# Performance work log

Hardware: AMD Instinct MI355X
Metric: run time of the kernel (lower is better)

Reference implementation:

```python
import jax, jax.numpy as jnp
import numpy as np

OUT_FEATURES = 4096
IN_FEATURES = 4096
NUMEL = OUT_FEATURES * IN_FEATURES          # 16777216
NUM_SUPER = NUMEL // 256                    # 65536 superblocks of 256 weights


def setup_inputs() -> dict:
    key = jax.random.key(0)
    k_x, k_p, k_d, k_dm, k_s, k_m = jax.random.split(key, 6)
    x = jax.random.normal(k_x, (2, 2048, IN_FEATURES), dtype=jnp.float32)
    # packed bytes: two 4-bit quants per byte
    packed = jax.random.randint(k_p, (NUMEL // 2,), 0, 256, dtype=jnp.int32)
    # per-superblock fp scale/min (small positive values like real Q4_K 'd'/'dmin')
    d = jax.random.uniform(k_d, (NUM_SUPER,), dtype=jnp.float32) * 0.02
    dmin = jax.random.uniform(k_dm, (NUM_SUPER,), dtype=jnp.float32) * 0.02
    # per-subblock 6-bit scale/min quants (8 subblocks per superblock)
    scales = jax.random.randint(k_s, (NUM_SUPER * 8,), 0, 64, dtype=jnp.int32)
    mins = jax.random.randint(k_m, (NUM_SUPER * 8,), 0, 64, dtype=jnp.int32)
    return {"x": x, "packed": packed, "d": d, "dmin": dmin,
            "scales": scales, "mins": mins}


def _q4_k_dequantize(packed, d, dmin, scales, mins):
    # nibble split: low then high, interleaved per byte (stack dim=1 + flatten)
    low = packed & 15
    high = (packed >> 4) & 15
    q = jnp.stack([low, high], axis=1).reshape(-1).astype(jnp.float32)  # [NUMEL]
    blocks = q.reshape(NUM_SUPER, 8, 32)
    blk_scale = (scales.astype(jnp.float32) / 63.0).reshape(NUM_SUPER, 8, 1)
    blk_min = (mins.astype(jnp.float32) / 63.0).reshape(NUM_SUPER, 8, 1)
    normalized = blocks / 15.0 * blk_scale + blk_min
    w = normalized * d.reshape(NUM_SUPER, 1, 1) + dmin.reshape(NUM_SUPER, 1, 1)
    return w.reshape(OUT_FEATURES, IN_FEATURES)


def reference(x, packed, d, dmin, scales, mins):
    w = _q4_k_dequantize(packed, d, dmin, scales, mins).astype(x.dtype)
    # F.linear(x, w) = x @ w.T ; bias is None
    return jnp.einsum('bsk,nk->bsn', x, w)
```

## Files before the change

kernel.cpp:

```cpp
#include <hip/hip_runtime.h>
#include <stdint.h>

#define M_DIM 4096
#define K_DIM 4096
#define N_DIM 4096

typedef float f32x4 __attribute__((ext_vector_type(4)));
typedef int   i32x4 __attribute__((ext_vector_type(4)));

__global__ __launch_bounds__(256) void quant_x(const float* __restrict__ x,
                                               int8_t* __restrict__ xq,
                                               float* __restrict__ sx) {
    __shared__ float red[4];
    const int row  = blockIdx.x;
    const int base = threadIdx.x * 16;
    const float* xr = x + (size_t)row * K_DIM + base;
    float4 v[4];
#pragma unroll
    for (int c = 0; c < 4; ++c) v[c] = ((const float4*)xr)[c];
    float am = 0.f;
#pragma unroll
    for (int c = 0; c < 4; ++c) {
        am = fmaxf(am, fabsf(v[c].x)); am = fmaxf(am, fabsf(v[c].y));
        am = fmaxf(am, fabsf(v[c].z)); am = fmaxf(am, fabsf(v[c].w));
    }
#pragma unroll
    for (int off = 32; off; off >>= 1) am = fmaxf(am, __shfl_xor(am, off, 64));
    if ((threadIdx.x & 63) == 0) red[threadIdx.x >> 6] = am;
    __syncthreads();
    float amax = fmaxf(fmaxf(red[0], red[1]), fmaxf(red[2], red[3]));
    amax = fmaxf(amax, 1e-20f);
    const float inv = 127.0f / amax;
    int ow[4];
#pragma unroll
    for (int c = 0; c < 4; ++c) {
        int q0 = __float2int_rn(v[c].x * inv);
        int q1 = __float2int_rn(v[c].y * inv);
        int q2 = __float2int_rn(v[c].z * inv);
        int q3 = __float2int_rn(v[c].w * inv);
        ow[c] = (q0 & 255) | ((q1 & 255) << 8) | ((q2 & 255) << 16) | ((q3 & 255) << 24);
    }
    ((int4*)(xq + (size_t)row * K_DIM + base))[0] = make_int4(ow[0], ow[1], ow[2], ow[3]);
    if (threadIdx.x == 0) sx[row] = amax / 127.0f;
}

__global__ __launch_bounds__(256) void quant_w(const int* __restrict__ packed,
                                               const float* __restrict__ d,
                                               const float* __restrict__ dmin,
                                               const int* __restrict__ scales,
                                               const int* __restrict__ mins,
                                               int8_t* __restrict__ wq,
                                               float* __restrict__ sw) {
    __shared__ float sa[128], sb[128], red[4];
    const int n = blockIdx.x;
    const int t = threadIdx.x;
    float m = 0.f;
    if (t < 128) {
        int sub  = n * 128 + t;
        int sidx = n * 16 + (t >> 3);
        float dd = d[sidx], dm = dmin[sidx];
        float a = dd * (float)scales[sub] * (1.0f / 945.0f);
        float b = dd * (float)mins[sub] * (1.0f / 63.0f) + dm;
        sa[t] = a; sb[t] = b;
        m = 15.0f * a + b;
    }
#pragma unroll
    for (int off = 32; off; off >>= 1) m = fmaxf(m, __shfl_xor(m, off, 64));
    if ((t & 63) == 0) red[t >> 6] = m;
    __syncthreads();
    float rowmax = fmaxf(fmaxf(red[0], red[1]), fmaxf(red[2], red[3]));
    rowmax = fmaxf(rowmax, 1e-20f);
    const float inv = 127.0f / rowmax;

    const int sub = t >> 1;
    const float a = sa[sub] * inv;
    const float b = sb[sub] * inv;
    const int4* p4 = (const int4*)(packed + (size_t)n * (K_DIM / 2) + t * 8);
    int4 pv0 = p4[0], pv1 = p4[1];
    int bytes[8] = {pv0.x, pv0.y, pv0.z, pv0.w, pv1.x, pv1.y, pv1.z, pv1.w};
    int ow[4];
#pragma unroll
    for (int c = 0; c < 4; ++c) {
        int b0 = bytes[2 * c], b1 = bytes[2 * c + 1];
        int q0 = __float2int_rn((float)(b0 & 15) * a + b);
        int q1 = __float2int_rn((float)((b0 >> 4) & 15) * a + b);
        int q2 = __float2int_rn((float)(b1 & 15) * a + b);
        int q3 = __float2int_rn((float)((b1 >> 4) & 15) * a + b);
        ow[c] = (q0 & 255) | ((q1 & 255) << 8) | ((q2 & 255) << 16) | ((q3 & 255) << 24);
    }
    ((int4*)(wq + (size_t)n * K_DIM + t * 16))[0] = make_int4(ow[0], ow[1], ow[2], ow[3]);
    if (t == 0) sw[n] = rowmax / 127.0f;
}

#define BM 128
#define BN 128
#define BKB 64

__device__ __forceinline__ void async_copy16(void* lds, const void* g) {
    __builtin_amdgcn_global_load_lds(
        (const __attribute__((address_space(1))) void*)g,
        (__attribute__((address_space(3))) void*)lds, 16, 0, 0);
}

__global__ __launch_bounds__(256) void gemm_i8(const int8_t* __restrict__ A,
                                               const int8_t* __restrict__ B,
                                               const float* __restrict__ sx,
                                               const float* __restrict__ sw,
                                               float* __restrict__ C) {
    __shared__ int8_t sAb[2][BM * BKB];
    __shared__ int8_t sBb[2][BN * BKB];

    const int tid  = threadIdx.x;
    const int wave = tid >> 6;
    const int lane = tid & 63;
    const int wm = wave >> 1;
    const int wn = wave & 1;
    const int r = lane & 15;
    const int q = lane >> 4;

    const int bid  = blockIdx.x;
    const int xcd  = bid & 7;
    const int slot = bid >> 3;
    const int m0 = (((xcd >> 2) << 4) + (slot & 15)) * BM;
    const int n0 = (((xcd & 3) << 3) + (slot >> 4)) * BN;

    i32x4 acc[4][4] = {};

    const int rowS = tid >> 2;
    const int kcS  = ((lane & 3) ^ ((lane >> 3) & 3)) * 16;
    const int8_t* gA0 = A + (size_t)(m0 + rowS) * K_DIM + kcS;
    const int8_t* gA1 = gA0 + (size_t)64 * K_DIM;
    const int8_t* gB0 = B + (size_t)(n0 + rowS) * K_DIM + kcS;
    const int8_t* gB1 = gB0 + (size_t)64 * K_DIM;
    const int ldsOff = wave * 1024;

    const int fragOff = (4 * r + (q ^ ((r >> 1) & 3))) * 16;

#define STAGE(buf, koff)                                                  \
    do {                                                                  \
        async_copy16(&sAb[buf][ldsOff],        gA0 + (koff));             \
        async_copy16(&sAb[buf][4096 + ldsOff], gA1 + (koff));             \
        async_copy16(&sBb[buf][ldsOff],        gB0 + (koff));             \
        async_copy16(&sBb[buf][4096 + ldsOff], gB1 + (koff));             \
    } while (0)

#define COMPUTE(buf)                                                      \
    do {                                                                  \
        i32x4 af[4], bfr[4];                                              \
        _Pragma("unroll")                                                 \
        for (int tt = 0; tt < 4; ++tt) {                                  \
            af[tt]  = *(const i32x4*)&sAb[buf][(wm * 4 + tt) * 1024 + fragOff]; \
            bfr[tt] = *(const i32x4*)&sBb[buf][(wn * 4 + tt) * 1024 + fragOff]; \
        }                                                                 \
        _Pragma("unroll")                                                 \
        for (int ii = 0; ii < 4; ++ii)                                    \
            _Pragma("unroll")                                             \
            for (int jj = 0; jj < 4; ++jj)                                \
                acc[ii][jj] = __builtin_amdgcn_mfma_i32_16x16x64_i8(      \
                    af[ii], bfr[jj], acc[ii][jj], 0, 0, 0);               \
    } while (0)

    STAGE(0, 0);

#pragma unroll 2
    for (int i = 0; i < 63; ++i) {
        const int cur = i & 1;
        STAGE(cur ^ 1, (i + 1) * BKB);
        asm volatile("s_waitcnt vmcnt(4)" ::: "memory");
        asm volatile("s_barrier" ::: "memory");
        COMPUTE(cur);
        asm volatile("s_waitcnt lgkmcnt(0)" ::: "memory");
        asm volatile("s_barrier" ::: "memory");
    }
    asm volatile("s_waitcnt vmcnt(0)" ::: "memory");
    asm volatile("s_barrier" ::: "memory");
    COMPUTE(1);

#pragma unroll
    for (int i = 0; i < 4; ++i) {
        int row = m0 + wm * 64 + i * 16 + q * 4;
#pragma unroll
        for (int j = 0; j < 4; ++j) {
            int col = n0 + wn * 64 + j * 16 + r;
            float swc = sw[col];
#pragma unroll
            for (int reg = 0; reg < 4; ++reg)
                C[(size_t)(row + reg) * N_DIM + col] =
                    (float)acc[i][j][reg] * sx[row + reg] * swc;
        }
    }
#undef STAGE
#undef COMPUTE
}

extern "C" void kernel_launch(void* const* d_in, const int* in_sizes, int n_in,
                              void* d_out, int out_size, void* d_ws, size_t ws_size,
                              hipStream_t stream) {
    const float* x      = (const float*)d_in[0];
    const int*   packed = (const int*)d_in[1];
    const float* d      = (const float*)d_in[2];
    const float* dmin   = (const float*)d_in[3];
    const int*   scales = (const int*)d_in[4];
    const int*   mins   = (const int*)d_in[5];
    float* out = (float*)d_out;

    int8_t* xq = (int8_t*)d_ws;
    int8_t* wq = xq + (size_t)M_DIM * K_DIM;
    float*  sx = (float*)(wq + (size_t)N_DIM * K_DIM);
    float*  sw = sx + M_DIM;

    quant_x<<<M_DIM, 256, 0, stream>>>(x, xq, sx);
    quant_w<<<N_DIM, 256, 0, stream>>>(packed, d, dmin, scales, mins, wq, sw);
    gemm_i8<<<1024, 256, 0, stream>>>(xq, wq, sx, sw, out);
}
```

Baseline: 250.1 us.

## Rewrite int8 GEMM as 256x256 tile with 8 waves and half-tile pipelining

Replaces the 128x128x64 int8 GEMM with a 256x256 output tile per 512-thread block. The tile is split into 128-row halves, and loads of each half are interleaved with MFMA on the others through a staged ping-pong schedule over BK=128 and an XOR-swizzled LDS layout. It adds s_setprio around the MFMA bursts and remaps block IDs across XCDs. The aim is more reuse per byte loaded and better overlap of global-to-LDS copies with compute, at the cost of 128KB of LDS, heavy register pressure and many barriers.

```diff
diff --git a/kernel.cpp b/kernel.cpp
--- a/kernel.cpp
+++ b/kernel.cpp
@@ -92,9 +92,7 @@
     if (t == 0) sw[n] = rowmax / 127.0f;
 }
 
-#define BM 128
-#define BN 128
-#define BKB 64
+#define BK 128
 
 __device__ __forceinline__ void async_copy16(void* lds, const void* g) {
     __builtin_amdgcn_global_load_lds(
@@ -102,95 +100,165 @@
         (__attribute__((address_space(3))) void*)lds, 16, 0, 0);
 }
 
-__global__ __launch_bounds__(256) void gemm_i8(const int8_t* __restrict__ A,
-                                               const int8_t* __restrict__ B,
-                                               const float* __restrict__ sx,
-                                               const float* __restrict__ sw,
-                                               float* __restrict__ C) {
-    __shared__ int8_t sAb[2][BM * BKB];
-    __shared__ int8_t sBb[2][BN * BKB];
+#define BARRIER() asm volatile("s_barrier" ::: "memory")
+#define LGKM0()   asm volatile("s_waitcnt lgkmcnt(0)" ::: "memory")
+#define WAITV(n)  asm volatile("s_waitcnt vmcnt(" #n ")" ::: "memory")
+
+__global__ __launch_bounds__(512, 2) void gemm_i8(const int8_t* __restrict__ A,
+                                                  const int8_t* __restrict__ B,
+                                                  const float* __restrict__ sx,
+                                                  const float* __restrict__ sw,
+                                                  float* __restrict__ C) {
+    __shared__ int8_t sA[2][2][128 * 128];
+    __shared__ int8_t sB[2][2][128 * 128];
 
     const int tid  = threadIdx.x;
     const int wave = tid >> 6;
     const int lane = tid & 63;
-    const int wm = wave >> 1;
-    const int wn = wave & 1;
-    const int r = lane & 15;
-    const int q = lane >> 4;
-
-    const int bid  = blockIdx.x;
-    const int xcd  = bid & 7;
-    const int slot = bid >> 3;
-    const int m0 = (((xcd >> 2) << 4) + (slot & 15)) * BM;
-    const int n0 = (((xcd & 3) << 3) + (slot >> 4)) * BN;
-
-    i32x4 acc[4][4] = {};
-
-    const int rowS = tid >> 2;
-    const int kcS  = ((lane & 3) ^ ((lane >> 3) & 3)) * 16;
-    const int8_t* gA0 = A + (size_t)(m0 + rowS) * K_DIM + kcS;
-    const int8_t* gA1 = gA0 + (size_t)64 * K_DIM;
-    const int8_t* gB0 = B + (size_t)(n0 + rowS) * K_DIM + kcS;
-    const int8_t* gB1 = gB0 + (size_t)64 * K_DIM;
-    const int ldsOff = wave * 1024;
-
-    const int fragOff = (4 * r + (q ^ ((r >> 1) & 3))) * 16;
-
-#define STAGE(buf, koff)                                                  \
-    do {                                                                  \
-        async_copy16(&sAb[buf][ldsOff],        gA0 + (koff));             \
-        async_copy16(&sAb[buf][4096 + ldsOff], gA1 + (koff));             \
-        async_copy16(&sBb[buf][ldsOff],        gB0 + (koff));             \
-        async_copy16(&sBb[buf][4096 + ldsOff], gB1 + (koff));             \
-    } while (0)
-
-#define COMPUTE(buf)                                                      \
-    do {                                                                  \
-        i32x4 af[4], bfr[4];                                              \
-        _Pragma("unroll")                                                 \
-        for (int tt = 0; tt < 4; ++tt) {                                  \
-            af[tt]  = *(const i32x4*)&sAb[buf][(wm * 4 + tt) * 1024 + fragOff]; \
-            bfr[tt] = *(const i32x4*)&sBb[buf][(wn * 4 + tt) * 1024 + fragOff]; \
+    const int wm = wave >> 2;
+    const int wn = wave & 3;
+    const int r4 = lane & 15;
+    const int q  = lane >> 4;
+
+    const int bid = blockIdx.x;
+    const int lid = (bid & 7) * 32 + (bid >> 3);
+    const int m0 = (lid & 15) * 256;
+    const int n0 = (lid >> 4) * 256;
+
+    i32x4 acc[2][2][4][2] = {};
+    i32x4 aF[2][4], bF[2][2];
+
+    const int rowS = tid >> 3;
+    const int cS   = (tid & 7) ^ (rowS & 7);
+    const size_t rs64 = (size_t)64 * K_DIM;
+    const int8_t* gAh[2];
+    const int8_t* gBh[2];
+    gAh[0] = A + (size_t)(m0 + rowS) * K_DIM + cS * 16;
+    gAh[1] = gAh[0] + (size_t)128 * K_DIM;
+    gBh[0] = B + (size_t)(n0 + rowS) * K_DIM + cS * 16;
+    gBh[1] = gBh[0] + (size_t)128 * K_DIM;
+    const int ldsW = wave * 1024;
+
+#define STAGE_A(buf, half, koff)                                          \
+    do {                                                                  \
+        async_copy16(&sA[buf][half][ldsW],        gAh[half] + (koff));    \
+        async_copy16(&sA[buf][half][ldsW + 8192], gAh[half] + rs64 + (koff)); \
+    } while (0)
+#define STAGE_B(buf, half, koff)                                          \
+    do {                                                                  \
+        async_copy16(&sB[buf][half][ldsW],        gBh[half] + (koff));    \
+        async_copy16(&sB[buf][half][ldsW + 8192], gBh[half] + rs64 + (koff)); \
+    } while (0)
+
+    int aOff[2][4], bOff[2][2];
+#pragma unroll
+    for (int ks = 0; ks < 2; ++ks) {
+        const int sl = (((ks * 4 + q) ^ (r4 & 7)) * 16);
+#pragma unroll
+        for (int m = 0; m < 4; ++m)
+            aOff[ks][m] = (wm * 64 + m * 16 + r4) * 128 + sl;
+#pragma unroll
+        for (int n = 0; n < 2; ++n)
+            bOff[ks][n] = (wn * 32 + n * 16 + r4) * 128 + sl;
+    }
+
+#define LDA(buf, half)                                                    \
+    do {                                                                  \
+        _Pragma("unroll") for (int ks = 0; ks < 2; ++ks)                  \
+        _Pragma("unroll") for (int m = 0; m < 4; ++m)                     \
+            aF[ks][m] = *(const i32x4*)&sA[buf][half][aOff[ks][m]];       \
+    } while (0)
+#define LDB(buf, half)                                                    \
+    do {                                                                  \
+        _Pragma("unroll") for (int ks = 0; ks < 2; ++ks)                  \
+        _Pragma("unroll") for (int n = 0; n < 2; ++n)                     \
+            bF[ks][n] = *(const i32x4*)&sB[buf][half][bOff[ks][n]];       \
+    } while (0)
+#define MMA(a, b)                                                         \
+    do {                                                                  \
+        __builtin_amdgcn_s_setprio(1);                                    \
+        _Pragma("unroll") for (int m = 0; m < 4; ++m)                     \
+        _Pragma("unroll") for (int n = 0; n < 2; ++n) {                   \
+            acc[a][b][m][n] = __builtin_amdgcn_mfma_i32_16x16x64_i8(      \
+                aF[0][m], bF[0][n], acc[a][b][m][n], 0, 0, 0);            \
+            acc[a][b][m][n] = __builtin_amdgcn_mfma_i32_16x16x64_i8(      \
+                aF[1][m], bF[1][n], acc[a][b][m][n], 0, 0, 0);            \
         }                                                                 \
-        _Pragma("unroll")                                                 \
-        for (int ii = 0; ii < 4; ++ii)                                    \
-            _Pragma("unroll")                                             \
-            for (int jj = 0; jj < 4; ++jj)                                \
-                acc[ii][jj] = __builtin_amdgcn_mfma_i32_16x16x64_i8(      \
-                    af[ii], bfr[jj], acc[ii][jj], 0, 0, 0);               \
-    } while (0)
-
-    STAGE(0, 0);
-
-#pragma unroll 2
-    for (int i = 0; i < 63; ++i) {
-        const int cur = i & 1;
-        STAGE(cur ^ 1, (i + 1) * BKB);
-        asm volatile("s_waitcnt vmcnt(4)" ::: "memory");
-        asm volatile("s_barrier" ::: "memory");
-        COMPUTE(cur);
-        asm volatile("s_waitcnt lgkmcnt(0)" ::: "memory");
-        asm volatile("s_barrier" ::: "memory");
-    }
-    asm volatile("s_waitcnt vmcnt(0)" ::: "memory");
-    asm volatile("s_barrier" ::: "memory");
-    COMPUTE(1);
-
-#pragma unroll
-    for (int i = 0; i < 4; ++i) {
-        int row = m0 + wm * 64 + i * 16 + q * 4;
-#pragma unroll
-        for (int j = 0; j < 4; ++j) {
-            int col = n0 + wn * 64 + j * 16 + r;
-            float swc = sw[col];
-#pragma unroll
-            for (int reg = 0; reg < 4; ++reg)
-                C[(size_t)(row + reg) * N_DIM + col] =
-                    (float)acc[i][j][reg] * sx[row + reg] * swc;
+        __builtin_amdgcn_s_setprio(0);                                    \
+    } while (0)
+
+    STAGE_A(0, 0, 0);
+    STAGE_B(0, 0, 0);
+    STAGE_B(0, 1, 0);
+    STAGE_A(0, 1, 0);
+    STAGE_A(1, 0, BK);
+    STAGE_B(1, 1, BK);
+    WAITV(4);
+    BARRIER();
+
+    int ko1 = BK, ko2 = 2 * BK, ko3 = 3 * BK;
+#pragma unroll 1
+    for (int it = 0; it < 15; ++it) {
+        LDA(0, 0); LDB(0, 0); STAGE_A(1, 1, ko1);
+        BARRIER(); LGKM0(); MMA(0, 0); BARRIER();
+        LDB(0, 1); STAGE_B(1, 0, ko1);
+        BARRIER(); LGKM0(); MMA(0, 1); BARRIER();
+        LDA(0, 1); STAGE_A(0, 0, ko2);
+        BARRIER(); LGKM0(); MMA(1, 1); BARRIER();
+        LDB(0, 0); STAGE_B(0, 1, ko2); WAITV(4);
+        BARRIER(); LGKM0(); MMA(1, 0); BARRIER();
+        LDA(1, 0); LDB(1, 0); STAGE_A(0, 1, ko2);
+        BARRIER(); LGKM0(); MMA(0, 0); BARRIER();
+        LDB(1, 1); STAGE_B(0, 0, ko2);
+        BARRIER(); LGKM0(); MMA(0, 1); BARRIER();
+        LDA(1, 1); STAGE_A(1, 0, ko3);
+        BARRIER(); LGKM0(); MMA(1, 1); BARRIER();
+        LDB(1, 0); STAGE_B(1, 1, ko3); WAITV(4);
+        BARRIER(); LGKM0(); MMA(1, 0); BARRIER();
+        ko1 += 2 * BK; ko2 += 2 * BK; ko3 += 2 * BK;
+    }
+
+    LDA(0, 0); LDB(0, 0); STAGE_A(1, 1, ko1);
+    BARRIER(); LGKM0(); MMA(0, 0); BARRIER();
+    LDB(0, 1); STAGE_B(1, 0, ko1);
+    BARRIER(); LGKM0(); MMA(0, 1); BARRIER();
+    LDA(0, 1);
+    BARRIER(); LGKM0(); MMA(1, 1); BARRIER();
+    LDB(0, 0); WAITV(0);
+    BARRIER(); LGKM0(); MMA(1, 0); BARRIER();
+    LDA(1, 0); LDB(1, 0);
+    BARRIER(); LGKM0(); MMA(0, 0); BARRIER();
+    LDB(1, 1);
+    BARRIER(); LGKM0(); MMA(0, 1); BARRIER();
+    LDA(1, 1);
+    BARRIER(); LGKM0(); MMA(1, 1); BARRIER();
+    LDB(1, 0);
+    BARRIER(); LGKM0(); MMA(1, 0);
+
+#pragma unroll
+    for (int a = 0; a < 2; ++a)
+#pragma unroll
+    for (int m = 0; m < 4; ++m) {
+        const int rbase = m0 + a * 128 + wm * 64 + m * 16 + q * 4;
+        const float4 s4 = *(const float4*)&sx[rbase];
+#pragma unroll
+        for (int b = 0; b < 2; ++b)
+#pragma unroll
+        for (int n = 0; n < 2; ++n) {
+            const int col = n0 + b * 128 + wn * 32 + n * 16 + r4;
+            const float swc = sw[col];
+            float* cp = C + (size_t)rbase * N_DIM + col;
+            cp[0 * N_DIM] = (float)acc[a][b][m][n][0] * s4.x * swc;
+            cp[1 * N_DIM] = (float)acc[a][b][m][n][1] * s4.y * swc;
+            cp[2 * N_DIM] = (float)acc[a][b][m][n][2] * s4.z * swc;
+            cp[3 * N_DIM] = (float)acc[a][b][m][n][3] * s4.w * swc;
         }
     }
-#undef STAGE
-#undef COMPUTE
+#undef STAGE_A
+#undef STAGE_B
+#undef LDA
+#undef LDB
+#undef MMA
 }
 
 extern "C" void kernel_launch(void* const* d_in, const int* in_sizes, int n_in,
@@ -211,5 +279,5 @@
 
     quant_x<<<M_DIM, 256, 0, stream>>>(x, xq, sx);
     quant_w<<<N_DIM, 256, 0, stream>>>(packed, d, dmin, scales, mins, wq, sw);
-    gemm_i8<<<1024, 256, 0, stream>>>(xq, wq, sx, sw, out);
-}
+    gemm_i8<<<256, 512, 0, stream>>>(xq, wq, sx, sw, out);
+}
```

After: 225.6 us. -9.8%, faster.

## Merge quantization kernels and enlarge GEMM tile to 128x256 with setprio

Applied to the files above, without the earlier changes.

Merges the x and weight quantization kernels into a single launch to cut one launch gap. The int8 GEMM tile grows from 128x128 to 128x256 per block, so each wave holds a 4x8 accumulator grid. The goal is more MFMA work per LDS fragment load and fewer blocks (512). The pipeline now waits on all loads before each barrier, uses s_setprio around the MFMA burst, and loads row scales with one vectorized read. Costs are more accumulator registers (lower occupancy) and only 512 blocks across the CUs.

```diff
diff --git a/kernel.cpp b/kernel.cpp
--- a/kernel.cpp
+++ b/kernel.cpp
@@ -8,185 +8,194 @@
 typedef float f32x4 __attribute__((ext_vector_type(4)));
 typedef int   i32x4 __attribute__((ext_vector_type(4)));
 
-__global__ __launch_bounds__(256) void quant_x(const float* __restrict__ x,
-                                               int8_t* __restrict__ xq,
-                                               float* __restrict__ sx) {
-    __shared__ float red[4];
-    const int row  = blockIdx.x;
-    const int base = threadIdx.x * 16;
-    const float* xr = x + (size_t)row * K_DIM + base;
-    float4 v[4];
-#pragma unroll
-    for (int c = 0; c < 4; ++c) v[c] = ((const float4*)xr)[c];
-    float am = 0.f;
-#pragma unroll
-    for (int c = 0; c < 4; ++c) {
-        am = fmaxf(am, fabsf(v[c].x)); am = fmaxf(am, fabsf(v[c].y));
-        am = fmaxf(am, fabsf(v[c].z)); am = fmaxf(am, fabsf(v[c].w));
-    }
-#pragma unroll
-    for (int off = 32; off; off >>= 1) am = fmaxf(am, __shfl_xor(am, off, 64));
-    if ((threadIdx.x & 63) == 0) red[threadIdx.x >> 6] = am;
-    __syncthreads();
-    float amax = fmaxf(fmaxf(red[0], red[1]), fmaxf(red[2], red[3]));
-    amax = fmaxf(amax, 1e-20f);
-    const float inv = 127.0f / amax;
-    int ow[4];
-#pragma unroll
-    for (int c = 0; c < 4; ++c) {
-        int q0 = __float2int_rn(v[c].x * inv);
-        int q1 = __float2int_rn(v[c].y * inv);
-        int q2 = __float2int_rn(v[c].z * inv);
-        int q3 = __float2int_rn(v[c].w * inv);
-        ow[c] = (q0 & 255) | ((q1 & 255) << 8) | ((q2 & 255) << 16) | ((q3 & 255) << 24);
-    }
-    ((int4*)(xq + (size_t)row * K_DIM + base))[0] = make_int4(ow[0], ow[1], ow[2], ow[3]);
-    if (threadIdx.x == 0) sx[row] = amax / 127.0f;
-}
-
-__global__ __launch_bounds__(256) void quant_w(const int* __restrict__ packed,
-                                               const float* __restrict__ d,
-                                               const float* __restrict__ dmin,
-                                               const int* __restrict__ scales,
-                                               const int* __restrict__ mins,
-                                               int8_t* __restrict__ wq,
-                                               float* __restrict__ sw) {
+__global__ __launch_bounds__(256) void quant_xw(const float* __restrict__ x,
+                                                const int* __restrict__ packed,
+                                                const float* __restrict__ d,
+                                                const float* __restrict__ dmin,
+                                                const int* __restrict__ scales,
+                                                const int* __restrict__ mins,
+                                                int8_t* __restrict__ xq,
+                                                float* __restrict__ sx,
+                                                int8_t* __restrict__ wq,
+                                                float* __restrict__ sw) {
     __shared__ float sa[128], sb[128], red[4];
-    const int n = blockIdx.x;
-    const int t = threadIdx.x;
-    float m = 0.f;
-    if (t < 128) {
-        int sub  = n * 128 + t;
-        int sidx = n * 16 + (t >> 3);
-        float dd = d[sidx], dm = dmin[sidx];
-        float a = dd * (float)scales[sub] * (1.0f / 945.0f);
-        float b = dd * (float)mins[sub] * (1.0f / 63.0f) + dm;
-        sa[t] = a; sb[t] = b;
-        m = 15.0f * a + b;
-    }
-#pragma unroll
-    for (int off = 32; off; off >>= 1) m = fmaxf(m, __shfl_xor(m, off, 64));
-    if ((t & 63) == 0) red[t >> 6] = m;
-    __syncthreads();
-    float rowmax = fmaxf(fmaxf(red[0], red[1]), fmaxf(red[2], red[3]));
-    rowmax = fmaxf(rowmax, 1e-20f);
-    const float inv = 127.0f / rowmax;
-
-    const int sub = t >> 1;
-    const float a = sa[sub] * inv;
-    const float b = sb[sub] * inv;
-    const int4* p4 = (const int4*)(packed + (size_t)n * (K_DIM / 2) + t * 8);
-    int4 pv0 = p4[0], pv1 = p4[1];
-    int bytes[8] = {pv0.x, pv0.y, pv0.z, pv0.w, pv1.x, pv1.y, pv1.z, pv1.w};
-    int ow[4];
-#pragma unroll
-    for (int c = 0; c < 4; ++c) {
-        int b0 = bytes[2 * c], b1 = bytes[2 * c + 1];
-        int q0 = __float2int_rn((float)(b0 & 15) * a + b);
-        int q1 = __float2int_rn((float)((b0 >> 4) & 15) * a + b);
-        int q2 = __float2int_rn((float)(b1 & 15) * a + b);
-        int q3 = __float2int_rn((float)((b1 >> 4) & 15) * a + b);
-        ow[c] = (q0 & 255) | ((q1 & 255) << 8) | ((q2 & 255) << 16) | ((q3 & 255) << 24);
-    }
-    ((int4*)(wq + (size_t)n * K_DIM + t * 16))[0] = make_int4(ow[0], ow[1], ow[2], ow[3]);
-    if (t == 0) sw[n] = rowmax / 127.0f;
-}
-
-#define BM 128
-#define BN 128
-#define BKB 64
+    if (blockIdx.x < 4096) {
+        const int row  = blockIdx.x;
+        const int base = threadIdx.x * 16;
+        const float* xr = x + (size_t)row * K_DIM + base;
+        float4 v[4];
+#pragma unroll
+        for (int c = 0; c < 4; ++c) v[c] = ((const float4*)xr)[c];
+        float am = 0.f;
+#pragma unroll
+        for (int c = 0; c < 4; ++c) {
+            am = fmaxf(am, fabsf(v[c].x)); am = fmaxf(am, fabsf(v[c].y));
+            am = fmaxf(am, fabsf(v[c].z)); am = fmaxf(am, fabsf(v[c].w));
+        }
+#pragma unroll
+        for (int off = 32; off; off >>= 1) am = fmaxf(am, __shfl_xor(am, off, 64));
+        if ((threadIdx.x & 63) == 0) red[threadIdx.x >> 6] = am;
+        __syncthreads();
+        float amax = fmaxf(fmaxf(red[0], red[1]), fmaxf(red[2], red[3]));
+        amax = fmaxf(amax, 1e-20f);
+        const float inv = 127.0f / amax;
+        int ow[4];
+#pragma unroll
+        for (int c = 0; c < 4; ++c) {
+            int q0 = __float2int_rn(v[c].x * inv);
+            int q1 = __float2int_rn(v[c].y * inv);
+            int q2 = __float2int_rn(v[c].z * inv);
+            int q3 = __float2int_rn(v[c].w * inv);
+            ow[c] = (q0 & 255) | ((q1 & 255) << 8) | ((q2 & 255) << 16) | ((q3 & 255) << 24);
+        }
+        ((int4*)(xq + (size_t)row * K_DIM + base))[0] = make_int4(ow[0], ow[1], ow[2], ow[3]);
+        if (threadIdx.x == 0) sx[row] = amax / 127.0f;
+    } else {
+        const int n = blockIdx.x - 4096;
+        const int t = threadIdx.x;
+        float m = 0.f;
+        if (t < 128) {
+            int sub  = n * 128 + t;
+            int sidx = n * 16 + (t >> 3);
+            float dd = d[sidx], dm = dmin[sidx];
+            float a = dd * (float)scales[sub] * (1.0f / 945.0f);
+            float b = dd * (float)mins[sub] * (1.0f / 63.0f) + dm;
+            sa[t] = a; sb[t] = b;
+            m = 15.0f * a + b;
+        }
+#pragma unroll
+        for (int off = 32; off; off >>= 1) m = fmaxf(m, __shfl_xor(m, off, 64));
+        if ((t & 63) == 0) red[t >> 6] = m;
+        __syncthreads();
+        float rowmax = fmaxf(fmaxf(red[0], red[1]), fmaxf(red[2], red[3]));
+        rowmax = fmaxf(rowmax, 1e-20f);
+        const float inv = 127.0f / rowmax;
+
+        const int sub = t >> 1;
+        const float a = sa[sub] * inv;
+        const float b = sb[sub] * inv;
+        const int4* p4 = (const int4*)(packed + (size_t)n * (K_DIM / 2) + t * 8);
+        int4 pv0 = p4[0], pv1 = p4[1];
+        int bytes[8] = {pv0.x, pv0.y, pv0.z, pv0.w, pv1.x, pv1.y, pv1.z, pv1.w};
+        int ow[4];
+#pragma unroll
+        for (int c = 0; c < 4; ++c) {
+            int b0 = bytes[2 * c], b1 = bytes[2 * c + 1];
+            int q0 = __float2int_rn((float)(b0 & 15) * a + b);
+            int q1 = __float2int_rn((float)((b0 >> 4) & 15) * a + b);
+            int q2 = __float2int_rn((float)(b1 & 15) * a + b);
+            int q3 = __float2int_rn((float)((b1 >> 4) & 15) * a + b);
+            ow[c] = (q0 & 255) | ((q1 & 255) << 8) | ((q2 & 255) << 16) | ((q3 & 255) << 24);
+        }
+        ((int4*)(wq + (size_t)n * K_DIM + t * 16))[0] = make_int4(ow[0], ow[1], ow[2], ow[3]);
+        if (t == 0) sw[n] = rowmax / 127.0f;
+    }
+}
+
+#define BK 64
 
 __device__ __forceinline__ void async_copy16(void* lds, const void* g) {
     __builtin_amdgcn_global_load_lds(
         (const __attribute__((address_space(1))) void*)g,
         (__attribute__((address_space(3))) void*)lds, 16, 0, 0);
 }
+
+#define BARRIER() asm volatile("s_barrier" ::: "memory")
+#define WAITV(n)  asm volatile("s_waitcnt vmcnt(" #n ")" ::: "memory")
+#define mfma64(a, b, c) __builtin_amdgcn_mfma_i32_16x16x64_i8(a, b, c, 0, 0, 0)
 
 __global__ __launch_bounds__(256) void gemm_i8(const int8_t* __restrict__ A,
                                                const int8_t* __restrict__ B,
                                                const float* __restrict__ sx,
                                                const float* __restrict__ sw,
                                                float* __restrict__ C) {
-    __shared__ int8_t sAb[2][BM * BKB];
-    __shared__ int8_t sBb[2][BN * BKB];
+    __shared__ int8_t sA[2][128 * 64];
+    __shared__ int8_t sB[2][256 * 64];
 
     const int tid  = threadIdx.x;
     const int wave = tid >> 6;
     const int lane = tid & 63;
     const int wm = wave >> 1;
     const int wn = wave & 1;
-    const int r = lane & 15;
-    const int q = lane >> 4;
-
-    const int bid  = blockIdx.x;
-    const int xcd  = bid & 7;
-    const int slot = bid >> 3;
-    const int m0 = (((xcd >> 2) << 4) + (slot & 15)) * BM;
-    const int n0 = (((xcd & 3) << 3) + (slot >> 4)) * BN;
-
-    i32x4 acc[4][4] = {};
+    const int r4 = lane & 15;
+    const int q  = lane >> 4;
+
+    const int bid = blockIdx.x;
+    const int lid = (bid & 7) * 64 + (bid >> 3);
+    const int m0 = (lid & 31) * 128;
+    const int n0 = (lid >> 5) * 256;
+
+    i32x4 acc[4][8] = {};
+    i32x4 aF[4], bF[8];
 
     const int rowS = tid >> 2;
-    const int kcS  = ((lane & 3) ^ ((lane >> 3) & 3)) * 16;
-    const int8_t* gA0 = A + (size_t)(m0 + rowS) * K_DIM + kcS;
-    const int8_t* gA1 = gA0 + (size_t)64 * K_DIM;
-    const int8_t* gB0 = B + (size_t)(n0 + rowS) * K_DIM + kcS;
-    const int8_t* gB1 = gB0 + (size_t)64 * K_DIM;
-    const int ldsOff = wave * 1024;
-
-    const int fragOff = (4 * r + (q ^ ((r >> 1) & 3))) * 16;
+    const int cS   = (tid & 3) ^ (rowS & 3);
+    const size_t rs64 = (size_t)64 * K_DIM;
+    const int8_t* gA = A + (size_t)(m0 + rowS) * K_DIM + cS * 16;
+    const int8_t* gB = B + (size_t)(n0 + rowS) * K_DIM + cS * 16;
+    const int ldsW = wave * 1024;
 
 #define STAGE(buf, koff)                                                  \
     do {                                                                  \
-        async_copy16(&sAb[buf][ldsOff],        gA0 + (koff));             \
-        async_copy16(&sAb[buf][4096 + ldsOff], gA1 + (koff));             \
-        async_copy16(&sBb[buf][ldsOff],        gB0 + (koff));             \
-        async_copy16(&sBb[buf][4096 + ldsOff], gB1 + (koff));             \
+        async_copy16(&sA[buf][ldsW],         gA + (koff));                \
+        async_copy16(&sA[buf][4096 + ldsW],  gA + rs64 + (koff));         \
+        async_copy16(&sB[buf][ldsW],         gB + (koff));                \
+        async_copy16(&sB[buf][4096 + ldsW],  gB + rs64 + (koff));         \
+        async_copy16(&sB[buf][8192 + ldsW],  gB + 2 * rs64 + (koff));     \
+        async_copy16(&sB[buf][12288 + ldsW], gB + 3 * rs64 + (koff));     \
     } while (0)
+
+    int aOff[4], bOff[8];
+    {
+        const int sl = (q ^ (r4 & 3)) * 16;
+#pragma unroll
+        for (int m = 0; m < 4; ++m)
+            aOff[m] = (wm * 64 + m * 16 + r4) * 64 + sl;
+#pragma unroll
+        for (int n = 0; n < 8; ++n)
+            bOff[n] = (wn * 128 + n * 16 + r4) * 64 + sl;
+    }
 
 #define COMPUTE(buf)                                                      \
     do {                                                                  \
-        i32x4 af[4], bfr[4];                                              \
-        _Pragma("unroll")                                                 \
-        for (int tt = 0; tt < 4; ++tt) {                                  \
-            af[tt]  = *(const i32x4*)&sAb[buf][(wm * 4 + tt) * 1024 + fragOff]; \
-            bfr[tt] = *(const i32x4*)&sBb[buf][(wn * 4 + tt) * 1024 + fragOff]; \
-        }                                                                 \
-        _Pragma("unroll")                                                 \
-        for (int ii = 0; ii < 4; ++ii)                                    \
-            _Pragma("unroll")                                             \
-            for (int jj = 0; jj < 4; ++jj)                                \
-                acc[ii][jj] = __builtin_amdgcn_mfma_i32_16x16x64_i8(      \
-                    af[ii], bfr[jj], acc[ii][jj], 0, 0, 0);               \
+        _Pragma("unroll") for (int m = 0; m < 4; ++m)                     \
+            aF[m] = *(const i32x4*)&sA[buf][aOff[m]];                     \
+        _Pragma("unroll") for (int n = 0; n < 8; ++n)                     \
+            bF[n] = *(const i32x4*)&sB[buf][bOff[n]];                     \
+        __builtin_amdgcn_s_setprio(1);                                    \
+        _Pragma("unroll") for (int n = 0; n < 8; ++n)                     \
+        _Pragma("unroll") for (int m = 0; m < 4; ++m)                     \
+            acc[m][n] = mfma64(aF[m], bF[n], acc[m][n]);                  \
+        __builtin_amdgcn_s_setprio(0);                                    \
     } while (0)
 
     STAGE(0, 0);
-
-#pragma unroll 2
-    for (int i = 0; i < 63; ++i) {
-        const int cur = i & 1;
-        STAGE(cur ^ 1, (i + 1) * BKB);
-        asm volatile("s_waitcnt vmcnt(4)" ::: "memory");
-        asm volatile("s_barrier" ::: "memory");
-        COMPUTE(cur);
-        asm volatile("s_waitcnt lgkmcnt(0)" ::: "memory");
-        asm volatile("s_barrier" ::: "memory");
-    }
-    asm volatile("s_waitcnt vmcnt(0)" ::: "memory");
-    asm volatile("s_barrier" ::: "memory");
+    WAITV(0);
+    BARRIER();
+
+#pragma unroll 1
+    for (int t = 0; t < 63; ++t) {
+        const int p = t & 1;
+        STAGE(p ^ 1, (t + 1) * BK);
+        COMPUTE(p);
+        WAITV(0);
+        BARRIER();
+    }
     COMPUTE(1);
 
 #pragma unroll
-    for (int i = 0; i < 4; ++i) {
-        int row = m0 + wm * 64 + i * 16 + q * 4;
-#pragma unroll
-        for (int j = 0; j < 4; ++j) {
-            int col = n0 + wn * 64 + j * 16 + r;
-            float swc = sw[col];
-#pragma unroll
-            for (int reg = 0; reg < 4; ++reg)
-                C[(size_t)(row + reg) * N_DIM + col] =
-                    (float)acc[i][j][reg] * sx[row + reg] * swc;
+    for (int m = 0; m < 4; ++m) {
+        const int rbase = m0 + wm * 64 + m * 16 + q * 4;
+        const float4 s4 = *(const float4*)&sx[rbase];
+#pragma unroll
+        for (int n = 0; n < 8; ++n) {
+            const int col = n0 + wn * 128 + n * 16 + r4;
+            const float swc = sw[col];
+            float* cp = C + (size_t)rbase * N_DIM + col;
+            cp[0 * N_DIM] = (float)acc[m][n][0] * s4.x * swc;
+            cp[1 * N_DIM] = (float)acc[m][n][1] * s4.y * swc;
+            cp[2 * N_DIM] = (float)acc[m][n][2] * s4.z * swc;
+            cp[3 * N_DIM] = (float)acc[m][n][3] * s4.w * swc;
         }
     }
 #undef STAGE
@@ -209,7 +218,7 @@
     float*  sx = (float*)(wq + (size_t)N_DIM * K_DIM);
     float*  sw = sx + M_DIM;
 
-    quant_x<<<M_DIM, 256, 0, stream>>>(x, xq, sx);
-    quant_w<<<N_DIM, 256, 0, stream>>>(packed, d, dmin, scales, mins, wq, sw);
-    gemm_i8<<<1024, 256, 0, stream>>>(xq, wq, sx, sw, out);
-}
+    quant_xw<<<8192, 256, 0, stream>>>(x, packed, d, dmin, scales, mins,
+                                       xq, sx, wq, sw);
+    gemm_i8<<<512, 256, 0, stream>>>(xq, wq, sx, sw, out);
+}
```

Result: faster. 236.5 us (-5.4%).
